# Performance work log

Hardware: AMD Instinct MI355X
Metric: run time of the kernel (lower is better)

The kernel has to match this reference:

```python
import jax, jax.numpy as jnp
import numpy as np

PATCH_SIZE = 128
NUM_PATCHES = 4


def setup_inputs() -> dict:
    key = jax.random.key(0)
    k1, k2 = jax.random.split(key)
    B, C, H, W = 32, 3, 512, 512
    images = jax.random.normal(k1, (B, C, H, W), dtype=jnp.float32)
    uncertainty_maps = jax.random.uniform(k2, (B, 1, H, W), dtype=jnp.float32)
    return {"images": images, "uncertainty_maps": uncertainty_maps}


def _select_patches(umap):
    """Greedy masked-argmax patch selection on one [H, W] uncertainty map.
    Returns coords [NUM_PATCHES, 4] int32 as (x1, y1, x2, y2)."""
    H, W = umap.shape
    eps = min(PATCH_SIZE, H // 2, W // 2)   # effective patch size (static)
    half = eps // 2
    margin = max(eps // 4, 1)
    ys = jnp.arange(H)[:, None]
    xs = jnp.arange(W)[None, :]

    def fix(a1, a2, L):
        # enforce window of exactly `eps` when clipped at the border
        small = (a2 - a1) < eps
        a2n = jnp.where(a1 == 0, jnp.minimum(L, a1 + eps), a2)
        a1n = jnp.where(a1 == 0, a1, jnp.maximum(0, a2 - eps))
        return jnp.where(small, a1n, a1), jnp.where(small, a2n, a2)

    def step(mask, _):
        masked = jnp.where(mask, -jnp.inf, umap)
        idx = jnp.argmax(masked)            # row-major first-max, same as np.ma.argmax
        yc = idx // W
        xc = idx % W
        x1 = jnp.maximum(0, xc - half)
        x2 = jnp.minimum(W, xc + half)
        y1 = jnp.maximum(0, yc - half)
        y2 = jnp.minimum(H, yc + half)
        x1, x2 = fix(x1, x2, W)
        y1, y2 = fix(y1, y2, H)
        # suppress selected region plus margin (clamping implicit in comparisons)
        box = (ys >= y1 - margin) & (ys < y2 + margin) & (xs >= x1 - margin) & (xs < x2 + margin)
        coords = jnp.stack([x1, y1, x2, y2]).astype(jnp.int32)
        return mask | box, coords

    _, coords = jax.lax.scan(step, jnp.zeros((H, W), dtype=bool), None, length=NUM_PATCHES)
    return coords  # [NUM_PATCHES, 4]


def _extract(images, coords):
    B, C, H, W = images.shape
    eps = min(PATCH_SIZE, H // 2, W // 2)

    def crop_one(img, c):
        # img [C,H,W], c = (x1,y1,x2,y2); window is always exactly eps x eps
        p = jax.lax.dynamic_slice(img, (0, c[1], c[0]), (C, eps, eps))
        if eps != PATCH_SIZE:
            # bilinear, matches F.interpolate(align_corners=False)
            p = jax.image.resize(p, (C, PATCH_SIZE, PATCH_SIZE), method="bilinear")
        return p

    return jax.vmap(jax.vmap(crop_one, in_axes=(None, 0)), in_axes=(0, 0))(images, coords)


def reference(images, uncertainty_maps):
    coords = jax.vmap(_select_patches)(uncertainty_maps[:, 0])   # [B, N, 4] int32
    patches = _extract(images, coords)                           # [B, N, C, P, P]
    return patches, coords.astype(jnp.float32)
```

## Files before the change

kernel.cpp:

```cpp
#include <hip/hip_runtime.h>
#include <math.h>
#include <float.h>

#define BN 32
#define CH 3
#define HH 512
#define WW 512
#define NP 4
#define EPS 128
#define HALF 64
#define MARGIN 32

#define NT 4096
#define PATCH_ELEMS (BN * NP * CH * EPS * EPS)
#define F4_PER_MAP (NP * CH * EPS * EPS / 4)
#define NSLICE 16
#define F4_PER_SLICE (F4_PER_MAP / NSLICE)
#define K2_NTHR 1024
#define K2_NBLK (BN * NSLICE)
#define K1_NTHR 256
#define K1_NBLK (BN * NT / K1_NTHR)

__global__ __launch_bounds__(K1_NTHR)
void tile_scan(const float* __restrict__ umaps, float2* __restrict__ tiles)
{
    const int g  = blockIdx.x * K1_NTHR + threadIdx.x;
    const int b  = g >> 12;
    const int t  = g & (NT - 1);
    const int tx = t & 63, ty = t >> 6;
    const float* __restrict__ um = umaps + (size_t)b * HH * WW;
    const int x0 = tx << 3, y0 = ty << 3;
    float bv = -INFINITY; int bi = 0x7fffffff;
    #pragma unroll
    for (int r = 0; r < 8; ++r) {
        const int rowbase = (y0 + r) * WW + x0;
        const float4 a = *(const float4*)(um + rowbase);
        const float4 c = *(const float4*)(um + rowbase + 4);
        if (a.x > bv) { bv = a.x; bi = rowbase + 0; }
        if (a.y > bv) { bv = a.y; bi = rowbase + 1; }
        if (a.z > bv) { bv = a.z; bi = rowbase + 2; }
        if (a.w > bv) { bv = a.w; bi = rowbase + 3; }
        if (c.x > bv) { bv = c.x; bi = rowbase + 4; }
        if (c.y > bv) { bv = c.y; bi = rowbase + 5; }
        if (c.z > bv) { bv = c.z; bi = rowbase + 6; }
        if (c.w > bv) { bv = c.w; bi = rowbase + 7; }
    }
    tiles[g] = make_float2(bv, __int_as_float(bi));
}

__global__ __launch_bounds__(K2_NTHR)
void select_extract(const float* __restrict__ images,
                    const float* __restrict__ umaps,
                    const float2* __restrict__ tiles,
                    float* __restrict__ out)
{
    const int tid   = threadIdx.x;
    const int lane  = tid & 63;
    const int wave  = tid >> 6;
    const int b     = blockIdx.x & (BN - 1);
    const int slice = blockIdx.x >> 5;
    const float* __restrict__ um = umaps + (size_t)b * HH * WW;
    float* coords_out = out + PATCH_ELEMS;

    __shared__ float2 tvi[NT];
    __shared__ int   boxes[NP][4];
    __shared__ float rv[16];
    __shared__ int   ri[16];
    __shared__ int   sx1[NP], sy1[NP];

    {
        const float4* __restrict__ src = (const float4*)(tiles + (size_t)b * NT);
        float4* dst = (float4*)tvi;
        dst[tid]        = src[tid];
        dst[tid + 1024] = src[tid + 1024];
    }
    if (tid < NP) {
        boxes[tid][0] = 0; boxes[tid][1] = 0; boxes[tid][2] = 0; boxes[tid][3] = 0;
    }
    __syncthreads();

    for (int k = 0; k < NP; ++k) {
        float bv = -INFINITY; int bi = 0x7fffffff;
        #pragma unroll
        for (int i = 0; i < 4; ++i) {
            const float2 e = tvi[tid + (i << 10)];
            const float v = e.x; const int x = __float_as_int(e.y);
            if (v > bv || (v == bv && x < bi)) { bv = v; bi = x; }
        }
        #pragma unroll
        for (int off = 32; off > 0; off >>= 1) {
            float ov = __shfl_down(bv, off);
            int   oi = __shfl_down(bi, off);
            if (ov > bv || (ov == bv && oi < bi)) { bv = ov; bi = oi; }
        }
        if (lane == 0) { rv[wave] = bv; ri[wave] = bi; }
        __syncthreads();

        if (tid == 0) {
            bv = rv[0]; bi = ri[0];
            #pragma unroll
            for (int w = 1; w < 16; ++w)
                if (rv[w] > bv || (rv[w] == bv && ri[w] < bi)) { bv = rv[w]; bi = ri[w]; }
            const int yc = bi >> 9, xc = bi & 511;
            int x1 = max(0, xc - HALF), x2 = min(WW, xc + HALF);
            int y1 = max(0, yc - HALF), y2 = min(HH, yc + HALF);
            if (x2 - x1 < EPS) { if (x1 == 0) x2 = EPS; else x1 = x2 - EPS; }
            if (y2 - y1 < EPS) { if (y1 == 0) y2 = EPS; else y1 = y2 - EPS; }
            boxes[k][0] = max(x1 - MARGIN, 0);
            boxes[k][1] = min(x2 + MARGIN, WW);
            boxes[k][2] = max(y1 - MARGIN, 0);
            boxes[k][3] = min(y2 + MARGIN, HH);
            sx1[k] = x1; sy1[k] = y1;

            if (slice == 0) {
                const int o = (b * NP + k) * 4;
                coords_out[o + 0] = (float)x1;
                coords_out[o + 1] = (float)y1;
                coords_out[o + 2] = (float)x2;
                coords_out[o + 3] = (float)y2;
            }
        }
        __syncthreads();

        if (k == NP - 1) break;

        const int ex1 = boxes[k][0], ex2 = boxes[k][1];
        const int ey1 = boxes[k][2], ey2 = boxes[k][3];
        const int tx1 = ex1 >> 3, tx2 = (ex2 - 1) >> 3;
        const int ty1 = ey1 >> 3, ty2 = (ey2 - 1) >> 3;
        const int wt  = tx2 - tx1 + 1;
        const int nt2 = wt * (ty2 - ty1 + 1);
        if (tid < nt2) {
            const int tx = tx1 + tid % wt;
            const int ty = ty1 + tid / wt;
            const int t  = (ty << 6) + tx;
            const int X1 = tx << 3, Y1 = ty << 3;
            if (X1 >= ex1 && X1 + 8 <= ex2 && Y1 >= ey1 && Y1 + 8 <= ey2) {
                tvi[t] = make_float2(-INFINITY, __int_as_float(0x7fffffff));
            } else {
                unsigned xm[NP]; int byl[NP], byh[NP];
                #pragma unroll
                for (int j = 0; j < NP; ++j) {
                    const int lo = min(max(boxes[j][0] - X1, 0), 8);
                    const int hi = min(max(boxes[j][1] - X1, 0), 8);
                    xm[j]  = (0xFFu << lo) & (0xFFu >> (8 - hi));
                    byl[j] = boxes[j][2]; byh[j] = boxes[j][3];
                }
                float nv = -INFINITY; int ni = 0x7fffffff;
                #pragma unroll
                for (int r = 0; r < 8; ++r) {
                    const int y = Y1 + r;
                    unsigned m8 = 0;
                    #pragma unroll
                    for (int j = 0; j < NP; ++j)
                        m8 |= (y >= byl[j] && y < byh[j]) ? xm[j] : 0u;
                    const int rowbase = y * WW + X1;
                    const float4 a = *(const float4*)(um + rowbase);
                    const float4 c = *(const float4*)(um + rowbase + 4);
                    const float vals[8] = {a.x, a.y, a.z, a.w, c.x, c.y, c.z, c.w};
                    #pragma unroll
                    for (int j2 = 0; j2 < 8; ++j2) {
                        if (!((m8 >> j2) & 1u) && vals[j2] > nv) { nv = vals[j2]; ni = rowbase + j2; }
                    }
                }
                tvi[t] = make_float2(nv, __int_as_float(ni));
            }
        }
        __syncthreads();
    }

    float4* __restrict__ out4 = (float4*)out;
    #pragma unroll
    for (int it = 0; it < 3; ++it) {
        const int il  = slice * F4_PER_SLICE + (it << 10) + tid;
        const int nc  = il >> 12;
        const int n   = nc / 3;
        const int c   = nc - n * 3;
        const int py  = (il >> 5) & 127;
        const int px0 = (il & 31) << 2;

        const int x1 = sx1[n], y1 = sy1[n];
        const float* __restrict__ src =
            images + (((size_t)b * CH + c) * HH + (y1 + py)) * WW + x1 + px0;
        out4[(size_t)b * F4_PER_MAP + il] = make_float4(src[0], src[1], src[2], src[3]);
    }
}

extern "C" void kernel_launch(void* const* d_in, const int* in_sizes, int n_in,
                              void* d_out, int out_size, void* d_ws, size_t ws_size,
                              hipStream_t stream) {
    const float* images = (const float*)d_in[0];
    const float* umaps  = (const float*)d_in[1];
    float* out          = (float*)d_out;
    float2* tiles       = (float2*)d_ws;

    tile_scan<<<K1_NBLK, K1_NTHR, 0, stream>>>(umaps, tiles);
    select_extract<<<K2_NBLK, K2_NTHR, 0, stream>>>(images, umaps, tiles, out);
}
```

Measured before the change: 199.0 us.

## Split selection and extraction into separate kernels to avoid redundant selection

Result: faster. 188.2 us (-5.4%).

```diff
diff --git a/kernel.cpp b/kernel.cpp
--- a/kernel.cpp
+++ b/kernel.cpp
@@ -16,10 +16,9 @@
 #define F4_PER_MAP (NP * CH * EPS * EPS / 4)
 #define NSLICE 16
 #define F4_PER_SLICE (F4_PER_MAP / NSLICE)
-#define K2_NTHR 1024
-#define K2_NBLK (BN * NSLICE)
 #define K1_NTHR 256
 #define K1_NBLK (BN * NT / K1_NTHR)
+#define EX_NBLK (BN * NSLICE)
 
 __global__ __launch_bounds__(K1_NTHR)
 void tile_scan(const float* __restrict__ umaps, float2* __restrict__ tiles)
@@ -48,17 +47,16 @@
     tiles[g] = make_float2(bv, __int_as_float(bi));
 }
 
-__global__ __launch_bounds__(K2_NTHR)
-void select_extract(const float* __restrict__ images,
-                    const float* __restrict__ umaps,
-                    const float2* __restrict__ tiles,
-                    float* __restrict__ out)
+__global__ __launch_bounds__(1024)
+void select_k(const float* __restrict__ umaps,
+              const float2* __restrict__ tiles,
+              float* __restrict__ out,
+              int2* __restrict__ sxy)
 {
     const int tid   = threadIdx.x;
     const int lane  = tid & 63;
     const int wave  = tid >> 6;
-    const int b     = blockIdx.x & (BN - 1);
-    const int slice = blockIdx.x >> 5;
+    const int b     = blockIdx.x;
     const float* __restrict__ um = umaps + (size_t)b * HH * WW;
     float* coords_out = out + PATCH_ELEMS;
 
@@ -66,7 +64,6 @@
     __shared__ int   boxes[NP][4];
     __shared__ float rv[16];
     __shared__ int   ri[16];
-    __shared__ int   sx1[NP], sy1[NP];
 
     {
         const float4* __restrict__ src = (const float4*)(tiles + (size_t)b * NT);
@@ -110,15 +107,13 @@
             boxes[k][1] = min(x2 + MARGIN, WW);
             boxes[k][2] = max(y1 - MARGIN, 0);
             boxes[k][3] = min(y2 + MARGIN, HH);
-            sx1[k] = x1; sy1[k] = y1;
-
-            if (slice == 0) {
-                const int o = (b * NP + k) * 4;
-                coords_out[o + 0] = (float)x1;
-                coords_out[o + 1] = (float)y1;
-                coords_out[o + 2] = (float)x2;
-                coords_out[o + 3] = (float)y2;
-            }
+
+            const int o = (b * NP + k) * 4;
+            coords_out[o + 0] = (float)x1;
+            coords_out[o + 1] = (float)y1;
+            coords_out[o + 2] = (float)x2;
+            coords_out[o + 3] = (float)y2;
+            sxy[b * NP + k] = make_int2(x1, y1);
         }
         __syncthreads();
 
@@ -168,8 +163,18 @@
         }
         __syncthreads();
     }
-
+}
+
+__global__ __launch_bounds__(1024)
+void extract_k(const float* __restrict__ images,
+               const int2* __restrict__ sxy,
+               float* __restrict__ out)
+{
+    const int tid   = threadIdx.x;
+    const int b     = blockIdx.x >> 4;
+    const int slice = blockIdx.x & (NSLICE - 1);
     float4* __restrict__ out4 = (float4*)out;
+
     #pragma unroll
     for (int it = 0; it < 3; ++it) {
         const int il  = slice * F4_PER_SLICE + (it << 10) + tid;
@@ -179,9 +184,9 @@
         const int py  = (il >> 5) & 127;
         const int px0 = (il & 31) << 2;
 
-        const int x1 = sx1[n], y1 = sy1[n];
+        const int2 xy = sxy[b * NP + n];
         const float* __restrict__ src =
-            images + (((size_t)b * CH + c) * HH + (y1 + py)) * WW + x1 + px0;
+            images + (((size_t)b * CH + c) * HH + (xy.y + py)) * WW + xy.x + px0;
         out4[(size_t)b * F4_PER_MAP + il] = make_float4(src[0], src[1], src[2], src[3]);
     }
 }
@@ -193,7 +198,9 @@
     const float* umaps  = (const float*)d_in[1];
     float* out          = (float*)d_out;
     float2* tiles       = (float2*)d_ws;
+    int2*   sxy         = (int2*)((char*)d_ws + (size_t)BN * NT * sizeof(float2));
 
     tile_scan<<<K1_NBLK, K1_NTHR, 0, stream>>>(umaps, tiles);
-    select_extract<<<K2_NBLK, K2_NTHR, 0, stream>>>(images, umaps, tiles, out);
-}
+    select_k<<<BN, 1024, 0, stream>>>(umaps, tiles, out, sxy);
+    extract_k<<<EX_NBLK, 1024, 0, stream>>>(images, sxy, out);
+}
```
